# Performance work log

Measured on AMD Instinct MI355X. Metric: run time of the kernel, lower is better.

The kernel has to match this reference:

```python
import jax, jax.numpy as jnp
import numpy as np

N_IN = 262144      # input points
N_OUT = 65536      # output voxels
NBR = 32           # neighbors per voxel (uniform ragged list here)
E = N_OUT * NBR    # total edges
CIN = 32
COUT = 32
K = 3 + 1          # kernel_size = [4,4,4]
KV = K * K * K     # 64 kernel bins
EPS = 1e-8


def window_poly6(r):
    # poly6 window on normalized distance r in [0,1]
    return jnp.clip(1.0 - r * r, 0.0, 1.0) ** 3


def ball_to_cube_radial(p):
    # radially map unit ball to unit cube [-1,1]^3 (Open3D 'ball_to_cube_radial')
    n2 = jnp.sqrt(jnp.sum(p * p, axis=-1, keepdims=True) + 1e-12)
    ninf = jnp.max(jnp.abs(p), axis=-1, keepdims=True)
    scale = jnp.where(ninf > 1e-8, n2 / jnp.maximum(ninf, 1e-8), 0.0)
    return jnp.clip(p * scale, -1.0, 1.0)


def setup_inputs() -> dict:
    key = jax.random.key(0)
    ks = jax.random.split(key, 8)
    feats = jax.random.normal(ks[0], (N_IN, CIN), jnp.float32)
    inp_points = jax.random.uniform(ks[1], (N_IN, 3), jnp.float32)
    out_points = jax.random.uniform(ks[2], (N_OUT, 3), jnp.float32)
    out_extents = jnp.array([0.2], jnp.float32)  # voxel size
    scale_compat = jax.random.uniform(ks[3], (E,), jnp.float32)
    neighbors_index = jax.random.randint(ks[4], (E,), 0, N_IN).astype(jnp.int64)
    neighbors_row_splits = (jnp.arange(N_OUT + 1) * NBR).astype(jnp.int64)
    neighbors_distance = jax.random.uniform(ks[5], (E,), jnp.float32)
    # learned params of the ContinuousConv: kernel [4,4,4,Cin,Cout] flattened, bias
    W = jax.random.normal(ks[6], (KV, CIN, COUT), jnp.float32) * 0.05
    bias = jnp.zeros((COUT,), jnp.float32)
    return dict(feats=feats, inp_points=inp_points, out_points=out_points,
                out_extents=out_extents, scale_compat=scale_compat,
                neighbors_index=neighbors_index,
                neighbors_row_splits=neighbors_row_splits,
                neighbors_distance=neighbors_distance, W=W, bias=bias)


def reference(feats, inp_points, out_points, out_extents, scale_compat,
              neighbors_index, neighbors_row_splits, neighbors_distance,
              W, bias):
    # edge -> output-voxel index from ragged row splits
    out_idx = jnp.searchsorted(neighbors_row_splits, jnp.arange(E), side='right') - 1
    # per-neighbor importance (the CConvAggregationBlock weighting)
    a = scale_compat * window_poly6(neighbors_distance)
    # relative positions normalized to the voxel extent (ball radius = extent/2)
    rel = (inp_points[neighbors_index] - out_points[out_idx]) * (2.0 / out_extents[0])
    cube = ball_to_cube_radial(rel)                      # [E,3] in [-1,1]
    u = jnp.clip((cube + 1.0) * 0.5 * (K - 1), 0.0, K - 1)
    i0 = jnp.clip(jnp.floor(u), 0.0, K - 2)
    t = u - i0                                           # trilinear fractions [E,3]
    i0 = i0.astype(jnp.int32)
    fg = feats[neighbors_index]                          # gathered features [E,Cin]
    # accumulate importance-weighted features into per-voxel kernel bins
    B = jnp.zeros((N_OUT * KV, CIN), feats.dtype)
    for dx in (0, 1):
        for dy in (0, 1):
            for dz in (0, 1):
                w = ((t[:, 0] if dx else 1.0 - t[:, 0]) *
                     (t[:, 1] if dy else 1.0 - t[:, 1]) *
                     (t[:, 2] if dz else 1.0 - t[:, 2]))
                kflat = ((i0[:, 0] + dx) * K + (i0[:, 1] + dy)) * K + (i0[:, 2] + dz)
                B = B.at[out_idx * KV + kflat].add((w * a)[:, None] * fg)
    # kernel contraction + importance normalization (normalize=True) + bias + relu
    y = jnp.einsum('nkc,kcd->nd', B.reshape(N_OUT, KV, CIN), W)
    denom = jax.ops.segment_sum(a, out_idx, num_segments=N_OUT)
    y = y / jnp.maximum(denom, EPS)[:, None] + bias
    return jax.nn.relu(y)
```

## Files before the change

kernel.cpp:

```cpp
#include <hip/hip_runtime.h>
#include <hip/hip_bf16.h>


typedef unsigned short u16;
typedef unsigned int   u32;
typedef __attribute__((ext_vector_type(4))) float f32x4;
typedef __attribute__((ext_vector_type(8))) short short8;

#define NOUT    65536
#define VX      4
#define THREADS 512
#define EPW     128
#define NWG     (NOUT / VX)
#define BSTRIDE 2052
#define VROWB   (BSTRIDE * 4)
#define BL_BYTES (VX * VROWB)

#define OFF_W   BL_BYTES
#define OFF_BCA (OFF_W + 8*EPW*4)
#define OFF_FB  (OFF_BCA + EPW*4)
#define OFF_DEN (OFF_FB + EPW*4)
#define SMEM_BYTES (OFF_DEN + 16)

__global__ void prep_w_kernel(const float* __restrict__ W,
                              u16* __restrict__ wpk) {
  int id  = blockIdx.x * 256 + threadIdx.x;
  int j   = id & 7;
  int l   = (id >> 3) & 63;
  int bin = (id >> 9) & 63;
  int tb  = id >> 15;
  int kap = (bin << 5) + ((l >> 4) << 3) + j;
  int d   = (l & 15) + ((tb >> 1) << 4);
  float w = W[kap * 32 + d];
  unsigned u = __float_as_uint(w);
  u16 val;
  if (tb & 1) {
    float rem = w - __uint_as_float(u & 0xFFFF0000u);
    val = (u16)(__float_as_uint(rem) >> 16);
  } else {
    val = (u16)(u >> 16);
  }
  wpk[id] = val;
}

__launch_bounds__(THREADS, 8)
__global__ void cconv_kernel(const float* __restrict__ feats,
                             const float* __restrict__ inp_points,
                             const float* __restrict__ out_points,
                             const float* __restrict__ out_extents,
                             const float* __restrict__ scale_compat,
                             const int*   __restrict__ nbr_idx,
                             const int*   __restrict__ row_splits,
                             const float* __restrict__ nbr_dist,
                             const float* __restrict__ bias,
                             const u16*   __restrict__ wpk,
                             float*       __restrict__ out) {
  extern __shared__ __align__(16) char smem[];
  float* wls   = (float*)(smem + OFF_W);
  float* Yp    = wls;
  u32*   bca   = (u32*)(smem + OFF_BCA);
  int*   fbase = (int*)(smem + OFF_FB);
  float* den   = (float*)(smem + OFF_DEN);

  const int tid  = threadIdx.x;
  const int wg   = blockIdx.x;
  const int lane = tid & 63;
  const int wv   = tid >> 6;

  if (tid < EPW) {
    const bool is64 = (row_splits[1] == 0);
    int e  = tid;
    int v  = e >> 5;
    int gv = (wg << 2) + v;
    int ge = (wg << 7) + e;
    int idx = nbr_idx[is64 ? (ge << 1) : ge];
    float dist = nbr_dist[ge];
    float sc   = scale_compat[ge];
    float om = 1.f - dist * dist;
    om = fminf(fmaxf(om, 0.f), 1.f);
    float a = sc * om * om * om;
    float inv = 2.f / out_extents[0];
    float ox = out_points[gv * 3 + 0];
    float oy = out_points[gv * 3 + 1];
    float oz = out_points[gv * 3 + 2];
    float rx = (inp_points[idx * 3 + 0] - ox) * inv;
    float ry = (inp_points[idx * 3 + 1] - oy) * inv;
    float rz = (inp_points[idx * 3 + 2] - oz) * inv;
    float n2   = sqrtf(rx * rx + ry * ry + rz * rz + 1e-12f);
    float ninf = fmaxf(fabsf(rx), fmaxf(fabsf(ry), fabsf(rz)));
    float scl  = (ninf > 1e-8f) ? (n2 / ninf) : 0.f;
    float cx = fminf(fmaxf(rx * scl, -1.f), 1.f);
    float cy = fminf(fmaxf(ry * scl, -1.f), 1.f);
    float cz = fminf(fmaxf(rz * scl, -1.f), 1.f);
    float ux = fminf(fmaxf((cx + 1.f) * 1.5f, 0.f), 3.f);
    float uy = fminf(fmaxf((cy + 1.f) * 1.5f, 0.f), 3.f);
    float uz = fminf(fmaxf((cz + 1.f) * 1.5f, 0.f), 3.f);
    float fx = fminf(floorf(ux), 2.f);
    float fy = fminf(floorf(uy), 2.f);
    float fz = fminf(floorf(uz), 2.f);
    float tx = ux - fx, ty = uy - fy, tz = uz - fz;
    int ix = (int)fx, iy = (int)fy, iz = (int)fz;
    float X1 = tx * a, X0 = a - X1;
    float Y1 = ty,     Y0 = 1.f - ty;
    float Z1 = tz,     Z0 = 1.f - tz;
    float p00 = X0 * Y0, p01 = X0 * Y1, p10 = X1 * Y0, p11 = X1 * Y1;
    float wc[8];
    wc[0] = p00 * Z0; wc[1] = p00 * Z1; wc[2] = p01 * Z0; wc[3] = p01 * Z1;
    wc[4] = p10 * Z0; wc[5] = p10 * Z1; wc[6] = p11 * Z0; wc[7] = p11 * Z1;
    int kb = (ix * 4 + iy) * 4 + iz;
    u32 bb = (u32)(v * VROWB + (kb << 7));
    int nc = 0; u32 mask = 0;
    #pragma unroll
    for (int k = 0; k < 8; ++k) {
      if (wc[k] != 0.f) {
        wls[nc * EPW + e] = wc[k];
        mask |= (1u << k);
        ++nc;
      }
    }
    bca[e]   = bb | (mask << 16) | ((u32)nc << 24);
    fbase[e] = idx << 5;
    float s = a;
    s += __shfl_xor(s, 1);
    s += __shfl_xor(s, 2);
    s += __shfl_xor(s, 4);
    s += __shfl_xor(s, 8);
    s += __shfl_xor(s, 16);
    if ((lane & 31) == 0) den[v] = s;
  }
  __syncthreads();

  {
    #pragma unroll
    for (int rd = 0; rd < 2; ++rd) {
      int t = (rd << 9) + tid;
      int r = t >> 3;
      int k = t & 7;
      const float* g = feats + fbase[r] + (k << 2);
      __builtin_amdgcn_global_load_lds(
          (const __attribute__((address_space(1))) void*)(const void*)g,
          (__attribute__((address_space(3))) void*)(void*)((float*)smem + (t << 2)),
          16, 0, 0);
    }
  }
  __syncthreads();

  const int c  = tid & 31;
  const int e0 = tid >> 5;
  float fg[8];
  {
    const float* fs = (const float*)smem;
    #pragma unroll
    for (int it = 0; it < 8; ++it)
      fg[it] = fs[(((it << 4) + e0) << 5) + c];
  }
  __syncthreads();

  {
    f32x4 z = {0.f, 0.f, 0.f, 0.f};
    for (int i = tid; i < (BL_BYTES / 16); i += THREADS)
      ((f32x4*)smem)[i] = z;
  }
  __syncthreads();

  {
    #pragma unroll
    for (int it = 0; it < 8; ++it) {
      int   e    = (it << 4) + e0;
      u32   m    = bca[e];
      u32   base = (m & 0xFFFFu) + ((u32)c << 2);
      u32   mask = (m >> 16) & 0xFFu;
      int   nc   = (int)(m >> 24);
      float f    = fg[it];
      for (int j = 0; j < nc; ++j) {
        float w = wls[j * EPW + e];
        int   k = __builtin_ctz(mask);
        mask &= mask - 1;
        u32 d = ((k & 1) << 7) | ((k & 2) << 8) | ((k & 4) << 9);
        atomicAdd((float*)(smem + base + d), w * f);
      }
    }
  }
  __syncthreads();

  f32x4 acc0 = {0.f, 0.f, 0.f, 0.f};
  f32x4 acc1 = {0.f, 0.f, 0.f, 0.f};
  {
    const short8* wp = (const short8*)wpk;
    int v16 = lane & 15;
    int q   = lane >> 4;
    const char* arow = smem + (size_t)(v16 & 3) * VROWB;
    #pragma unroll
    for (int b = 0; b < 8; ++b) {
      int bin = (wv << 3) + b;
      short8 w0h = wp[((0 * 64 + bin) << 6) + lane];
      short8 w0l = wp[((1 * 64 + bin) << 6) + lane];
      short8 w1h = wp[((2 * 64 + bin) << 6) + lane];
      short8 w1l = wp[((3 * 64 + bin) << 6) + lane];
      const float* ap = (const float*)(arow + (bin << 7) + (q << 5));
      f32x4 a0 = *(const f32x4*)ap;
      f32x4 a1 = *(const f32x4*)(ap + 4);
      short8 ahi, alo;
      #pragma unroll
      for (int j = 0; j < 4; ++j) {
        unsigned u0 = __float_as_uint(a0[j]);
        ahi[j] = (short)(u0 >> 16);
        float r0 = a0[j] - __uint_as_float(u0 & 0xFFFF0000u);
        alo[j] = (short)(__float_as_uint(r0) >> 16);
        unsigned u1 = __float_as_uint(a1[j]);
        ahi[j + 4] = (short)(u1 >> 16);
        float r1 = a1[j] - __uint_as_float(u1 & 0xFFFF0000u);
        alo[j + 4] = (short)(__float_as_uint(r1) >> 16);
      }
      acc0 = __builtin_amdgcn_mfma_f32_16x16x32_bf16(ahi, w0h, acc0, 0, 0, 0);
      acc0 = __builtin_amdgcn_mfma_f32_16x16x32_bf16(ahi, w0l, acc0, 0, 0, 0);
      acc0 = __builtin_amdgcn_mfma_f32_16x16x32_bf16(alo, w0h, acc0, 0, 0, 0);
      acc1 = __builtin_amdgcn_mfma_f32_16x16x32_bf16(ahi, w1h, acc1, 0, 0, 0);
      acc1 = __builtin_amdgcn_mfma_f32_16x16x32_bf16(ahi, w1l, acc1, 0, 0, 0);
      acc1 = __builtin_amdgcn_mfma_f32_16x16x32_bf16(alo, w1h, acc1, 0, 0, 0);
    }
  }

  if (lane < 16) {
    float* yp = Yp + (wv << 7);
    #pragma unroll
    for (int r = 0; r < 4; ++r) {
      yp[r * 32 + lane]      = acc0[r];
      yp[r * 32 + 16 + lane] = acc1[r];
    }
  }
  __syncthreads();

  if (tid < EPW) {
    float s = 0.f;
    #pragma unroll
    for (int w = 0; w < 8; ++w) s += Yp[(w << 7) + tid];
    int v = tid >> 5;
    int d = tid & 31;
    float dn = fmaxf(den[v], 1e-8f);
    float y = s / dn + bias[d];
    out[(wg << 7) + tid] = fmaxf(y, 0.f);
  }
}

extern "C" void kernel_launch(void* const* d_in, const int* in_sizes, int n_in,
                              void* d_out, int out_size, void* d_ws, size_t ws_size,
                              hipStream_t stream) {
  const float* feats        = (const float*)d_in[0];
  const float* inp_points   = (const float*)d_in[1];
  const float* out_points   = (const float*)d_in[2];
  const float* out_extents  = (const float*)d_in[3];
  const float* scale_compat = (const float*)d_in[4];
  const int*   nbr_idx      = (const int*)d_in[5];
  const int*   row_splits   = (const int*)d_in[6];
  const float* nbr_dist     = (const float*)d_in[7];
  const float* W            = (const float*)d_in[8];
  const float* bias         = (const float*)d_in[9];

  u16* wpk = (u16*)d_ws;

  static_assert(SMEM_BYTES <= 40960, "LDS over 4-per-CU budget");
  (void)hipFuncSetAttribute((const void*)cconv_kernel,
                            hipFuncAttributeMaxDynamicSharedMemorySize,
                            SMEM_BYTES);

  prep_w_kernel<<<512, 256, 0, stream>>>(W, wpk);
  cconv_kernel<<<NWG, THREADS, SMEM_BYTES, stream>>>(
      feats, inp_points, out_points, out_extents, scale_compat, nbr_idx,
      row_splits, nbr_dist, bias, wpk, (float*)d_out);
}
```

Measured before the change: 625.2 us.

## Gather neighbor features from an FP16 copy to halve gather traffic

Result: no change. 628.7 us (+0.6%).

```diff
diff --git a/kernel.cpp b/kernel.cpp
--- a/kernel.cpp
+++ b/kernel.cpp
@@ -1,5 +1,6 @@
 #include <hip/hip_runtime.h>
 #include <hip/hip_bf16.h>
+#include <hip/hip_fp16.h>
 
 
 typedef unsigned short u16;
@@ -12,6 +13,7 @@
 #define THREADS 512
 #define EPW     128
 #define NWG     (NOUT / VX)
+#define NWG_SLOW 512
 #define BSTRIDE 2052
 #define VROWB   (BSTRIDE * 4)
 #define BL_BYTES (VX * VROWB)
@@ -21,6 +23,9 @@
 #define OFF_FB  (OFF_BCA + EPW*4)
 #define OFF_DEN (OFF_FB + EPW*4)
 #define SMEM_BYTES (OFF_DEN + 16)
+
+#define N_IN     262144
+#define FH_ELEMS (N_IN * 32)
 
 __global__ void prep_w_kernel(const float* __restrict__ W,
                               u16* __restrict__ wpk) {
@@ -43,18 +48,34 @@
   wpk[id] = val;
 }
 
+__global__ void prep_f_kernel(const float* __restrict__ F,
+                              __half* __restrict__ Fh) {
+  int i = blockIdx.x * 256 + threadIdx.x;
+  f32x4 v = ((const f32x4*)F)[i];
+  ushort4 h;
+  h.x = __half_as_ushort(__float2half(v[0]));
+  h.y = __half_as_ushort(__float2half(v[1]));
+  h.z = __half_as_ushort(__float2half(v[2]));
+  h.w = __half_as_ushort(__float2half(v[3]));
+  ((ushort4*)Fh)[i] = h;
+}
+
+template <bool FP16F, bool SLOWW>
 __launch_bounds__(THREADS, 8)
-__global__ void cconv_kernel(const float* __restrict__ feats,
-                             const float* __restrict__ inp_points,
-                             const float* __restrict__ out_points,
-                             const float* __restrict__ out_extents,
-                             const float* __restrict__ scale_compat,
-                             const int*   __restrict__ nbr_idx,
-                             const int*   __restrict__ row_splits,
-                             const float* __restrict__ nbr_dist,
-                             const float* __restrict__ bias,
-                             const u16*   __restrict__ wpk,
-                             float*       __restrict__ out) {
+__global__ void cconv_kernel(const float*  __restrict__ feats,
+                             const __half* __restrict__ feats_h,
+                             const float*  __restrict__ inp_points,
+                             const float*  __restrict__ out_points,
+                             const float*  __restrict__ out_extents,
+                             const float*  __restrict__ scale_compat,
+                             const int*    __restrict__ nbr_idx,
+                             const int*    __restrict__ row_splits,
+                             const float*  __restrict__ nbr_dist,
+                             const float*  __restrict__ bias,
+                             const u16*    __restrict__ wpk,
+                             const float*  __restrict__ W,
+                             float*        __restrict__ out,
+                             int wg_base) {
   extern __shared__ __align__(16) char smem[];
   float* wls   = (float*)(smem + OFF_W);
   float* Yp    = wls;
@@ -63,7 +84,7 @@
   float* den   = (float*)(smem + OFF_DEN);
 
   const int tid  = threadIdx.x;
-  const int wg   = blockIdx.x;
+  const int wg   = wg_base + blockIdx.x;
   const int lane = tid & 63;
   const int wv   = tid >> 6;
 
@@ -119,7 +140,7 @@
       }
     }
     bca[e]   = bb | (mask << 16) | ((u32)nc << 24);
-    fbase[e] = idx << 5;
+    fbase[e] = idx;
     float s = a;
     s += __shfl_xor(s, 1);
     s += __shfl_xor(s, 2);
@@ -130,16 +151,24 @@
   }
   __syncthreads();
 
-  {
+  if (FP16F) {
+    int r = tid >> 2;
+    int k = tid & 3;
+    const __half* g = feats_h + ((size_t)fbase[r] << 5) + (k << 3);
+    __builtin_amdgcn_global_load_lds(
+        (const __attribute__((address_space(1))) void*)(const void*)g,
+        (__attribute__((address_space(3))) void*)(void*)(smem + (tid << 4)),
+        16, 0, 0);
+  } else {
     #pragma unroll
     for (int rd = 0; rd < 2; ++rd) {
       int t = (rd << 9) + tid;
       int r = t >> 3;
       int k = t & 7;
-      const float* g = feats + fbase[r] + (k << 2);
+      const float* g = feats + ((size_t)fbase[r] << 5) + (k << 2);
       __builtin_amdgcn_global_load_lds(
           (const __attribute__((address_space(1))) void*)(const void*)g,
-          (__attribute__((address_space(3))) void*)(void*)((float*)smem + (t << 2)),
+          (__attribute__((address_space(3))) void*)(void*)(smem + (t << 4)),
           16, 0, 0);
     }
   }
@@ -148,7 +177,12 @@
   const int c  = tid & 31;
   const int e0 = tid >> 5;
   float fg[8];
-  {
+  if (FP16F) {
+    const __half* fs = (const __half*)smem;
+    #pragma unroll
+    for (int it = 0; it < 8; ++it)
+      fg[it] = __half2float(fs[(((it << 4) + e0) << 5) + c]);
+  } else {
     const float* fs = (const float*)smem;
     #pragma unroll
     for (int it = 0; it < 8; ++it)
@@ -193,10 +227,28 @@
     #pragma unroll
     for (int b = 0; b < 8; ++b) {
       int bin = (wv << 3) + b;
-      short8 w0h = wp[((0 * 64 + bin) << 6) + lane];
-      short8 w0l = wp[((1 * 64 + bin) << 6) + lane];
-      short8 w1h = wp[((2 * 64 + bin) << 6) + lane];
-      short8 w1l = wp[((3 * 64 + bin) << 6) + lane];
+      short8 w0h, w0l, w1h, w1l;
+      if (!SLOWW) {
+        w0h = wp[((0 * 64 + bin) << 6) + lane];
+        w0l = wp[((1 * 64 + bin) << 6) + lane];
+        w1h = wp[((2 * 64 + bin) << 6) + lane];
+        w1l = wp[((3 * 64 + bin) << 6) + lane];
+      } else {
+        #pragma unroll
+        for (int j = 0; j < 8; ++j) {
+          int kap = (bin << 5) + (q << 3) + j;
+          float f0 = W[kap * 32 + v16];
+          float f1 = W[kap * 32 + v16 + 16];
+          unsigned u0 = __float_as_uint(f0);
+          w0h[j] = (short)(u0 >> 16);
+          float r0 = f0 - __uint_as_float(u0 & 0xFFFF0000u);
+          w0l[j] = (short)(__float_as_uint(r0) >> 16);
+          unsigned u1 = __float_as_uint(f1);
+          w1h[j] = (short)(u1 >> 16);
+          float r1 = f1 - __uint_as_float(u1 & 0xFFFF0000u);
+          w1l[j] = (short)(__float_as_uint(r1) >> 16);
+        }
+      }
       const float* ap = (const float*)(arow + (bin << 7) + (q << 5));
       f32x4 a0 = *(const f32x4*)ap;
       f32x4 a1 = *(const f32x4*)(ap + 4);
@@ -256,16 +308,43 @@
   const float* nbr_dist     = (const float*)d_in[7];
   const float* W            = (const float*)d_in[8];
   const float* bias         = (const float*)d_in[9];
-
-  u16* wpk = (u16*)d_ws;
-
-  static_assert(SMEM_BYTES <= 40960, "LDS over 4-per-CU budget");
-  (void)hipFuncSetAttribute((const void*)cconv_kernel,
-                            hipFuncAttributeMaxDynamicSharedMemorySize,
-                            SMEM_BYTES);
-
-  prep_w_kernel<<<512, 256, 0, stream>>>(W, wpk);
-  cconv_kernel<<<NWG, THREADS, SMEM_BYTES, stream>>>(
-      feats, inp_points, out_points, out_extents, scale_compat, nbr_idx,
-      row_splits, nbr_dist, bias, wpk, (float*)d_out);
+  float*       outp         = (float*)d_out;
+
+  const size_t FH_BYTES  = (size_t)FH_ELEMS * 2;
+  const size_t WPK_BYTES = 262144;
+
+  (void)hipFuncSetAttribute((const void*)cconv_kernel<true, false>,
+                            hipFuncAttributeMaxDynamicSharedMemorySize, SMEM_BYTES);
+  (void)hipFuncSetAttribute((const void*)cconv_kernel<true, true>,
+                            hipFuncAttributeMaxDynamicSharedMemorySize, SMEM_BYTES);
+  (void)hipFuncSetAttribute((const void*)cconv_kernel<false, false>,
+                            hipFuncAttributeMaxDynamicSharedMemorySize, SMEM_BYTES);
+
+  if (ws_size >= FH_BYTES + WPK_BYTES) {
+    __half* feats_h = (__half*)d_ws;
+    u16*    wpk     = (u16*)((char*)d_ws + FH_BYTES);
+    prep_f_kernel<<<FH_ELEMS / 4 / 256, 256, 0, stream>>>(feats, feats_h);
+    prep_w_kernel<<<512, 256, 0, stream>>>(W, wpk);
+    cconv_kernel<true, false><<<NWG, THREADS, SMEM_BYTES, stream>>>(
+        feats, feats_h, inp_points, out_points, out_extents, scale_compat,
+        nbr_idx, row_splits, nbr_dist, bias, wpk, W, outp, 0);
+  } else if (ws_size >= FH_BYTES) {
+    __half* feats_h = (__half*)d_ws;
+    u16*    wpk     = (u16*)((char*)d_out + (size_t)out_size * 4 - WPK_BYTES);
+    prep_f_kernel<<<FH_ELEMS / 4 / 256, 256, 0, stream>>>(feats, feats_h);
+    prep_w_kernel<<<512, 256, 0, stream>>>(W, wpk);
+    cconv_kernel<true, false><<<NWG - NWG_SLOW, THREADS, SMEM_BYTES, stream>>>(
+        feats, feats_h, inp_points, out_points, out_extents, scale_compat,
+        nbr_idx, row_splits, nbr_dist, bias, wpk, W, outp, 0);
+    cconv_kernel<true, true><<<NWG_SLOW, THREADS, SMEM_BYTES, stream>>>(
+        feats, feats_h, inp_points, out_points, out_extents, scale_compat,
+        nbr_idx, row_splits, nbr_dist, bias, (const u16*)nullptr, W, outp,
+        NWG - NWG_SLOW);
+  } else {
+    u16* wpk = (u16*)d_ws;
+    prep_w_kernel<<<512, 256, 0, stream>>>(W, wpk);
+    cconv_kernel<false, false><<<NWG, THREADS, SMEM_BYTES, stream>>>(
+        feats, (const __half*)nullptr, inp_points, out_points, out_extents,
+        scale_compat, nbr_idx, row_splits, nbr_dist, bias, wpk, W, outp, 0);
+  }
 }
```

## Make cconv kernel persistent with double-buffered geometry and feature gather prefetch

Applied to the files above, without the earlier changes.

Measured after the change: 707.2 us. +13.1%, slower.

```diff
diff --git a/kernel.cpp b/kernel.cpp
--- a/kernel.cpp
+++ b/kernel.cpp
@@ -11,16 +11,30 @@
 #define VX      4
 #define THREADS 512
 #define EPW     128
-#define NWG     (NOUT / VX)
+#define NGRP    (NOUT / VX)
+#define GRID    512
+#define GP      (NGRP / GRID)
 #define BSTRIDE 2052
 #define VROWB   (BSTRIDE * 4)
 #define BL_BYTES (VX * VROWB)
 
-#define OFF_W   BL_BYTES
-#define OFF_BCA (OFF_W + 8*EPW*4)
-#define OFF_FB  (OFF_BCA + EPW*4)
-#define OFF_DEN (OFF_FB + EPW*4)
-#define SMEM_BYTES (OFF_DEN + 16)
+#define OFF_FS0  BL_BYTES
+#define OFF_FS1  (OFF_FS0 + 16384)
+#define OFF_WL0  (OFF_FS1 + 16384)
+#define OFF_WL1  (OFF_WL0 + 4096)
+#define OFF_BC0  (OFF_WL1 + 4096)
+#define OFF_BC1  (OFF_BC0 + 512)
+#define OFF_FB0  (OFF_BC1 + 512)
+#define OFF_FB1  (OFF_FB0 + 512)
+#define OFF_DN0  (OFF_FB1 + 512)
+#define OFF_DN1  (OFF_DN0 + 16)
+#define SMEM_BYTES (OFF_DN1 + 16)
+
+#define LGKM_BAR() do {                                        \
+    asm volatile("s_waitcnt lgkmcnt(0)" ::: "memory");         \
+    __builtin_amdgcn_sched_barrier(0);                         \
+    __builtin_amdgcn_s_barrier();                              \
+  } while (0)
 
 __global__ void prep_w_kernel(const float* __restrict__ W,
                               u16* __restrict__ wpk) {
@@ -43,7 +57,73 @@
   wpk[id] = val;
 }
 
-__launch_bounds__(THREADS, 8)
+__device__ __forceinline__ void geom_phase(
+    int gid, int tid, int lane,
+    const float* inp_points, const float* out_points, float inv,
+    const float* scale_compat, const int* nbr_idx, bool is64,
+    const float* nbr_dist,
+    float* wlsq, u32* bcaq, int* fbq, float* denq) {
+  if (tid >= EPW) return;
+  int e  = tid;
+  int v  = e >> 5;
+  int gv = (gid << 2) + v;
+  int ge = (gid << 7) + e;
+  int idx = nbr_idx[is64 ? (ge << 1) : ge];
+  float dist = nbr_dist[ge];
+  float sc   = scale_compat[ge];
+  float om = 1.f - dist * dist;
+  om = fminf(fmaxf(om, 0.f), 1.f);
+  float a = sc * om * om * om;
+  float ox = out_points[gv * 3 + 0];
+  float oy = out_points[gv * 3 + 1];
+  float oz = out_points[gv * 3 + 2];
+  float rx = (inp_points[idx * 3 + 0] - ox) * inv;
+  float ry = (inp_points[idx * 3 + 1] - oy) * inv;
+  float rz = (inp_points[idx * 3 + 2] - oz) * inv;
+  float n2   = sqrtf(rx * rx + ry * ry + rz * rz + 1e-12f);
+  float ninf = fmaxf(fabsf(rx), fmaxf(fabsf(ry), fabsf(rz)));
+  float scl  = (ninf > 1e-8f) ? (n2 / ninf) : 0.f;
+  float cx = fminf(fmaxf(rx * scl, -1.f), 1.f);
+  float cy = fminf(fmaxf(ry * scl, -1.f), 1.f);
+  float cz = fminf(fmaxf(rz * scl, -1.f), 1.f);
+  float ux = fminf(fmaxf((cx + 1.f) * 1.5f, 0.f), 3.f);
+  float uy = fminf(fmaxf((cy + 1.f) * 1.5f, 0.f), 3.f);
+  float uz = fminf(fmaxf((cz + 1.f) * 1.5f, 0.f), 3.f);
+  float fx = fminf(floorf(ux), 2.f);
+  float fy = fminf(floorf(uy), 2.f);
+  float fz = fminf(floorf(uz), 2.f);
+  float tx = ux - fx, ty = uy - fy, tz = uz - fz;
+  int ix = (int)fx, iy = (int)fy, iz = (int)fz;
+  float X1 = tx * a, X0 = a - X1;
+  float Y1 = ty,     Y0 = 1.f - ty;
+  float Z1 = tz,     Z0 = 1.f - tz;
+  float p00 = X0 * Y0, p01 = X0 * Y1, p10 = X1 * Y0, p11 = X1 * Y1;
+  float wc[8];
+  wc[0] = p00 * Z0; wc[1] = p00 * Z1; wc[2] = p01 * Z0; wc[3] = p01 * Z1;
+  wc[4] = p10 * Z0; wc[5] = p10 * Z1; wc[6] = p11 * Z0; wc[7] = p11 * Z1;
+  int kb = (ix * 4 + iy) * 4 + iz;
+  u32 bb = (u32)(v * VROWB + (kb << 7));
+  int nc = 0; u32 mask = 0;
+  #pragma unroll
+  for (int k = 0; k < 8; ++k) {
+    if (wc[k] != 0.f) {
+      wlsq[nc * EPW + e] = wc[k];
+      mask |= (1u << k);
+      ++nc;
+    }
+  }
+  bcaq[e] = bb | (mask << 16) | ((u32)nc << 24);
+  fbq[e]  = idx;
+  float s = a;
+  s += __shfl_xor(s, 1);
+  s += __shfl_xor(s, 2);
+  s += __shfl_xor(s, 4);
+  s += __shfl_xor(s, 8);
+  s += __shfl_xor(s, 16);
+  if ((lane & 31) == 0) denq[v] = s;
+}
+
+__launch_bounds__(THREADS, 4)
 __global__ void cconv_kernel(const float* __restrict__ feats,
                              const float* __restrict__ inp_points,
                              const float* __restrict__ out_points,
@@ -56,190 +136,167 @@
                              const u16*   __restrict__ wpk,
                              float*       __restrict__ out) {
   extern __shared__ __align__(16) char smem[];
-  float* wls   = (float*)(smem + OFF_W);
-  float* Yp    = wls;
-  u32*   bca   = (u32*)(smem + OFF_BCA);
-  int*   fbase = (int*)(smem + OFF_FB);
-  float* den   = (float*)(smem + OFF_DEN);
 
   const int tid  = threadIdx.x;
-  const int wg   = blockIdx.x;
+  const int bid  = blockIdx.x;
   const int lane = tid & 63;
   const int wv   = tid >> 6;
-
-  if (tid < EPW) {
-    const bool is64 = (row_splits[1] == 0);
-    int e  = tid;
-    int v  = e >> 5;
-    int gv = (wg << 2) + v;
-    int ge = (wg << 7) + e;
-    int idx = nbr_idx[is64 ? (ge << 1) : ge];
-    float dist = nbr_dist[ge];
-    float sc   = scale_compat[ge];
-    float om = 1.f - dist * dist;
-    om = fminf(fmaxf(om, 0.f), 1.f);
-    float a = sc * om * om * om;
-    float inv = 2.f / out_extents[0];
-    float ox = out_points[gv * 3 + 0];
-    float oy = out_points[gv * 3 + 1];
-    float oz = out_points[gv * 3 + 2];
-    float rx = (inp_points[idx * 3 + 0] - ox) * inv;
-    float ry = (inp_points[idx * 3 + 1] - oy) * inv;
-    float rz = (inp_points[idx * 3 + 2] - oz) * inv;
-    float n2   = sqrtf(rx * rx + ry * ry + rz * rz + 1e-12f);
-    float ninf = fmaxf(fabsf(rx), fmaxf(fabsf(ry), fabsf(rz)));
-    float scl  = (ninf > 1e-8f) ? (n2 / ninf) : 0.f;
-    float cx = fminf(fmaxf(rx * scl, -1.f), 1.f);
-    float cy = fminf(fmaxf(ry * scl, -1.f), 1.f);
-    float cz = fminf(fmaxf(rz * scl, -1.f), 1.f);
-    float ux = fminf(fmaxf((cx + 1.f) * 1.5f, 0.f), 3.f);
-    float uy = fminf(fmaxf((cy + 1.f) * 1.5f, 0.f), 3.f);
-    float uz = fminf(fmaxf((cz + 1.f) * 1.5f, 0.f), 3.f);
-    float fx = fminf(floorf(ux), 2.f);
-    float fy = fminf(floorf(uy), 2.f);
-    float fz = fminf(floorf(uz), 2.f);
-    float tx = ux - fx, ty = uy - fy, tz = uz - fz;
-    int ix = (int)fx, iy = (int)fy, iz = (int)fz;
-    float X1 = tx * a, X0 = a - X1;
-    float Y1 = ty,     Y0 = 1.f - ty;
-    float Z1 = tz,     Z0 = 1.f - tz;
-    float p00 = X0 * Y0, p01 = X0 * Y1, p10 = X1 * Y0, p11 = X1 * Y1;
-    float wc[8];
-    wc[0] = p00 * Z0; wc[1] = p00 * Z1; wc[2] = p01 * Z0; wc[3] = p01 * Z1;
-    wc[4] = p10 * Z0; wc[5] = p10 * Z1; wc[6] = p11 * Z0; wc[7] = p11 * Z1;
-    int kb = (ix * 4 + iy) * 4 + iz;
-    u32 bb = (u32)(v * VROWB + (kb << 7));
-    int nc = 0; u32 mask = 0;
-    #pragma unroll
-    for (int k = 0; k < 8; ++k) {
-      if (wc[k] != 0.f) {
-        wls[nc * EPW + e] = wc[k];
-        mask |= (1u << k);
-        ++nc;
-      }
-    }
-    bca[e]   = bb | (mask << 16) | ((u32)nc << 24);
-    fbase[e] = idx << 5;
-    float s = a;
-    s += __shfl_xor(s, 1);
-    s += __shfl_xor(s, 2);
-    s += __shfl_xor(s, 4);
-    s += __shfl_xor(s, 8);
-    s += __shfl_xor(s, 16);
-    if ((lane & 31) == 0) den[v] = s;
-  }
+  const bool is64 = (row_splits[1] == 0);
+  const float inv = 2.f / out_extents[0];
+  const int c  = tid & 31;
+  const int e0 = tid >> 5;
+
+  geom_phase(bid, tid, lane, inp_points, out_points, inv, scale_compat,
+             nbr_idx, is64, nbr_dist,
+             (float*)(smem + OFF_WL0), (u32*)(smem + OFF_BC0),
+             (int*)(smem + OFF_FB0), (float*)(smem + OFF_DN0));
   __syncthreads();
-
   {
+    const int* fb0 = (const int*)(smem + OFF_FB0);
     #pragma unroll
     for (int rd = 0; rd < 2; ++rd) {
       int t = (rd << 9) + tid;
       int r = t >> 3;
       int k = t & 7;
-      const float* g = feats + fbase[r] + (k << 2);
+      const float* g = feats + ((size_t)fb0[r] << 5) + (k << 2);
       __builtin_amdgcn_global_load_lds(
           (const __attribute__((address_space(1))) void*)(const void*)g,
-          (__attribute__((address_space(3))) void*)(void*)((float*)smem + (t << 2)),
+          (__attribute__((address_space(3))) void*)(void*)(smem + OFF_FS0 + (t << 4)),
           16, 0, 0);
     }
   }
-  __syncthreads();
-
-  const int c  = tid & 31;
-  const int e0 = tid >> 5;
-  float fg[8];
-  {
-    const float* fs = (const float*)smem;
-    #pragma unroll
-    for (int it = 0; it < 8; ++it)
-      fg[it] = fs[(((it << 4) + e0) << 5) + c];
-  }
-  __syncthreads();
-
-  {
-    f32x4 z = {0.f, 0.f, 0.f, 0.f};
-    for (int i = tid; i < (BL_BYTES / 16); i += THREADS)
-      ((f32x4*)smem)[i] = z;
-  }
-  __syncthreads();
-
-  {
-    #pragma unroll
-    for (int it = 0; it < 8; ++it) {
-      int   e    = (it << 4) + e0;
-      u32   m    = bca[e];
-      u32   base = (m & 0xFFFFu) + ((u32)c << 2);
-      u32   mask = (m >> 16) & 0xFFu;
-      int   nc   = (int)(m >> 24);
-      float f    = fg[it];
-      for (int j = 0; j < nc; ++j) {
-        float w = wls[j * EPW + e];
-        int   k = __builtin_ctz(mask);
-        mask &= mask - 1;
-        u32 d = ((k & 1) << 7) | ((k & 2) << 8) | ((k & 4) << 9);
-        atomicAdd((float*)(smem + base + d), w * f);
+
+  int p = 0;
+  for (int it2 = 0; it2 < GP; ++it2) {
+    const int gid = it2 * GRID + bid;
+    const int q   = p ^ 1;
+    char* fs_p = smem + (p ? OFF_FS1 : OFF_FS0);
+    char* fs_q = smem + (q ? OFF_FS1 : OFF_FS0);
+    float* wls_p = (float*)(smem + (p ? OFF_WL1 : OFF_WL0));
+    float* Yp    = wls_p;
+    u32*  bca_p  = (u32*)(smem + (p ? OFF_BC1 : OFF_BC0));
+    float* den_p = (float*)(smem + (p ? OFF_DN1 : OFF_DN0));
+
+    __syncthreads();
+
+    float fg[8];
+    {
+      const float* fs = (const float*)fs_p;
+      #pragma unroll
+      for (int it = 0; it < 8; ++it)
+        fg[it] = fs[(((it << 4) + e0) << 5) + c];
+    }
+
+    if (it2 + 1 < GP) {
+      geom_phase(gid + GRID, tid, lane, inp_points, out_points, inv,
+                 scale_compat, nbr_idx, is64, nbr_dist,
+                 (float*)(smem + (q ? OFF_WL1 : OFF_WL0)),
+                 (u32*)(smem + (q ? OFF_BC1 : OFF_BC0)),
+                 (int*)(smem + (q ? OFF_FB1 : OFF_FB0)),
+                 (float*)(smem + (q ? OFF_DN1 : OFF_DN0)));
+    }
+    __syncthreads();
+
+    if (it2 + 1 < GP) {
+      const int* fbq = (const int*)(smem + (q ? OFF_FB1 : OFF_FB0));
+      #pragma unroll
+      for (int rd = 0; rd < 2; ++rd) {
+        int t = (rd << 9) + tid;
+        int r = t >> 3;
+        int k = t & 7;
+        const float* g = feats + ((size_t)fbq[r] << 5) + (k << 2);
+        __builtin_amdgcn_global_load_lds(
+            (const __attribute__((address_space(1))) void*)(const void*)g,
+            (__attribute__((address_space(3))) void*)(void*)(fs_q + (t << 4)),
+            16, 0, 0);
       }
     }
-  }
-  __syncthreads();
-
-  f32x4 acc0 = {0.f, 0.f, 0.f, 0.f};
-  f32x4 acc1 = {0.f, 0.f, 0.f, 0.f};
-  {
-    const short8* wp = (const short8*)wpk;
-    int v16 = lane & 15;
-    int q   = lane >> 4;
-    const char* arow = smem + (size_t)(v16 & 3) * VROWB;
-    #pragma unroll
-    for (int b = 0; b < 8; ++b) {
-      int bin = (wv << 3) + b;
-      short8 w0h = wp[((0 * 64 + bin) << 6) + lane];
-      short8 w0l = wp[((1 * 64 + bin) << 6) + lane];
-      short8 w1h = wp[((2 * 64 + bin) << 6) + lane];
-      short8 w1l = wp[((3 * 64 + bin) << 6) + lane];
-      const float* ap = (const float*)(arow + (bin << 7) + (q << 5));
-      f32x4 a0 = *(const f32x4*)ap;
-      f32x4 a1 = *(const f32x4*)(ap + 4);
-      short8 ahi, alo;
-      #pragma unroll
-      for (int j = 0; j < 4; ++j) {
-        unsigned u0 = __float_as_uint(a0[j]);
-        ahi[j] = (short)(u0 >> 16);
-        float r0 = a0[j] - __uint_as_float(u0 & 0xFFFF0000u);
-        alo[j] = (short)(__float_as_uint(r0) >> 16);
-        unsigned u1 = __float_as_uint(a1[j]);
-        ahi[j + 4] = (short)(u1 >> 16);
-        float r1 = a1[j] - __uint_as_float(u1 & 0xFFFF0000u);
-        alo[j + 4] = (short)(__float_as_uint(r1) >> 16);
+
+    {
+      f32x4 z = {0.f, 0.f, 0.f, 0.f};
+      for (int i = tid; i < (BL_BYTES / 16); i += THREADS)
+        ((f32x4*)smem)[i] = z;
+    }
+    LGKM_BAR();
+
+    {
+      #pragma unroll
+      for (int it = 0; it < 8; ++it) {
+        int   e    = (it << 4) + e0;
+        u32   m    = bca_p[e];
+        u32   base = (m & 0xFFFFu) + ((u32)c << 2);
+        u32   mask = (m >> 16) & 0xFFu;
+        int   nc   = (int)(m >> 24);
+        float f    = fg[it];
+        for (int j = 0; j < nc; ++j) {
+          float w = wls_p[j * EPW + e];
+          int   k = __builtin_ctz(mask);
+          mask &= mask - 1;
+          u32 d = ((k & 1) << 7) | ((k & 2) << 8) | ((k & 4) << 9);
+          atomicAdd((float*)(smem + base + d), w * f);
+        }
       }
-      acc0 = __builtin_amdgcn_mfma_f32_16x16x32_bf16(ahi, w0h, acc0, 0, 0, 0);
-      acc0 = __builtin_amdgcn_mfma_f32_16x16x32_bf16(ahi, w0l, acc0, 0, 0, 0);
-      acc0 = __builtin_amdgcn_mfma_f32_16x16x32_bf16(alo, w0h, acc0, 0, 0, 0);
-      acc1 = __builtin_amdgcn_mfma_f32_16x16x32_bf16(ahi, w1h, acc1, 0, 0, 0);
-      acc1 = __builtin_amdgcn_mfma_f32_16x16x32_bf16(ahi, w1l, acc1, 0, 0, 0);
-      acc1 = __builtin_amdgcn_mfma_f32_16x16x32_bf16(alo, w1h, acc1, 0, 0, 0);
-    }
-  }
-
-  if (lane < 16) {
-    float* yp = Yp + (wv << 7);
-    #pragma unroll
-    for (int r = 0; r < 4; ++r) {
-      yp[r * 32 + lane]      = acc0[r];
-      yp[r * 32 + 16 + lane] = acc1[r];
-    }
-  }
-  __syncthreads();
-
-  if (tid < EPW) {
-    float s = 0.f;
-    #pragma unroll
-    for (int w = 0; w < 8; ++w) s += Yp[(w << 7) + tid];
-    int v = tid >> 5;
-    int d = tid & 31;
-    float dn = fmaxf(den[v], 1e-8f);
-    float y = s / dn + bias[d];
-    out[(wg << 7) + tid] = fmaxf(y, 0.f);
+    }
+    LGKM_BAR();
+
+    f32x4 acc0 = {0.f, 0.f, 0.f, 0.f};
+    f32x4 acc1 = {0.f, 0.f, 0.f, 0.f};
+    {
+      const short8* wp = (const short8*)wpk;
+      int v16 = lane & 15;
+      int qq  = lane >> 4;
+      const char* arow = smem + (size_t)(v16 & 3) * VROWB;
+      #pragma unroll
+      for (int b = 0; b < 8; ++b) {
+        int bin = (wv << 3) + b;
+        short8 w0h = wp[((0 * 64 + bin) << 6) + lane];
+        short8 w0l = wp[((1 * 64 + bin) << 6) + lane];
+        short8 w1h = wp[((2 * 64 + bin) << 6) + lane];
+        short8 w1l = wp[((3 * 64 + bin) << 6) + lane];
+        const float* ap = (const float*)(arow + (bin << 7) + (qq << 5));
+        f32x4 a0 = *(const f32x4*)ap;
+        f32x4 a1 = *(const f32x4*)(ap + 4);
+        short8 ahi, alo;
+        #pragma unroll
+        for (int j = 0; j < 4; ++j) {
+          unsigned u0 = __float_as_uint(a0[j]);
+          ahi[j] = (short)(u0 >> 16);
+          float r0 = a0[j] - __uint_as_float(u0 & 0xFFFF0000u);
+          alo[j] = (short)(__float_as_uint(r0) >> 16);
+          unsigned u1 = __float_as_uint(a1[j]);
+          ahi[j + 4] = (short)(u1 >> 16);
+          float r1 = a1[j] - __uint_as_float(u1 & 0xFFFF0000u);
+          alo[j + 4] = (short)(__float_as_uint(r1) >> 16);
+        }
+        acc0 = __builtin_amdgcn_mfma_f32_16x16x32_bf16(ahi, w0h, acc0, 0, 0, 0);
+        acc0 = __builtin_amdgcn_mfma_f32_16x16x32_bf16(ahi, w0l, acc0, 0, 0, 0);
+        acc0 = __builtin_amdgcn_mfma_f32_16x16x32_bf16(alo, w0h, acc0, 0, 0, 0);
+        acc1 = __builtin_amdgcn_mfma_f32_16x16x32_bf16(ahi, w1h, acc1, 0, 0, 0);
+        acc1 = __builtin_amdgcn_mfma_f32_16x16x32_bf16(ahi, w1l, acc1, 0, 0, 0);
+        acc1 = __builtin_amdgcn_mfma_f32_16x16x32_bf16(alo, w1h, acc1, 0, 0, 0);
+      }
+    }
+
+    if (lane < 16) {
+      float* yp = Yp + (wv << 7);
+      #pragma unroll
+      for (int r = 0; r < 4; ++r) {
+        yp[r * 32 + lane]      = acc0[r];
+        yp[r * 32 + 16 + lane] = acc1[r];
+      }
+    }
+    LGKM_BAR();
+    if (tid < EPW) {
+      float s = 0.f;
+      #pragma unroll
+      for (int w = 0; w < 8; ++w) s += Yp[(w << 7) + tid];
+      int v = tid >> 5;
+      int d = tid & 31;
+      float dn = fmaxf(den_p[v], 1e-8f);
+      float y = s / dn + bias[d];
+      out[(gid << 7) + tid] = fmaxf(y, 0.f);
+    }
+    p = q;
   }
 }
 
@@ -259,13 +316,13 @@
 
   u16* wpk = (u16*)d_ws;
 
-  static_assert(SMEM_BYTES <= 40960, "LDS over 4-per-CU budget");
+  static_assert(SMEM_BYTES <= 81920, "LDS over 2-per-CU budget");
   (void)hipFuncSetAttribute((const void*)cconv_kernel,
                             hipFuncAttributeMaxDynamicSharedMemorySize,
                             SMEM_BYTES);
 
   prep_w_kernel<<<512, 256, 0, stream>>>(W, wpk);
-  cconv_kernel<<<NWG, THREADS, SMEM_BYTES, stream>>>(
+  cconv_kernel<<<GRID, THREADS, SMEM_BYTES, stream>>>(
       feats, inp_points, out_points, out_extents, scale_compat, nbr_idx,
       row_splits, nbr_dist, bias, wpk, (float*)d_out);
 }
```
